# Optimization experiments

Measured on AMD Instinct MI355X. Metric: run time of the kernel, lower is better.

## Reference

```python
import jax, jax.numpy as jnp
import numpy as np

B, T, C, H = 8, 2048, 1024, 64  # batch, seq, n_embed, head_size


def setup_inputs() -> dict:
    key = jax.random.key(0)
    ks = jax.random.split(key, 6)
    k = jax.random.normal(ks[0], (B, T, C), dtype=jnp.float32)
    q = jax.random.normal(ks[1], (B, T, C), dtype=jnp.float32)
    v = jax.random.normal(ks[2], (B, T, C), dtype=jnp.float32)
    mask = jnp.ones((B, T), dtype=jnp.int32)  # key-padding mask (1 = keep)
    # nn.Linear(n_embed, head_size, bias=False) weights: [head_size, n_embed]
    s = 1.0 / np.sqrt(C)
    Wk = jax.random.uniform(ks[3], (H, C), jnp.float32, -s, s)
    Wq = jax.random.uniform(ks[4], (H, C), jnp.float32, -s, s)
    Wv = jax.random.uniform(ks[5], (H, C), jnp.float32, -s, s)
    return {"k": k, "q": q, "v": v, "mask": mask, "Wk": Wk, "Wq": Wq, "Wv": Wv}


def reference(k, q, v, mask, Wk, Wq, Wv):
    Tq = q.shape[1]
    kh = jnp.einsum('btc,hc->bth', k, Wk)   # [B,T,H]
    qh = jnp.einsum('btc,hc->bth', q, Wq)   # [B,T,H]
    vh = jnp.einsum('btc,hc->bth', v, Wv)   # [B,T,H]
    scale = kh.shape[-1] ** -0.5
    wei = jnp.einsum('bqh,bkh->bqk', qh, kh) * scale  # [B,T,T]
    # causal (tril) mask
    tril = jnp.tril(jnp.ones((Tq, Tq), dtype=bool))
    neg_inf = jnp.finfo(wei.dtype).min
    wei = jnp.where(tril[None, :, :], wei, neg_inf)
    # key-padding mask: mask [B,T] -> broadcast over query rows
    wei = jnp.where(mask[:, None, :] != 0, wei, neg_inf)
    wei = jax.nn.softmax(wei, axis=-1)
    # dropout p=0.0 (eval) -> identity
    out = jnp.einsum('bqk,bkh->bqh', wei, vh)  # [B,T,H]
    return out
```

## Files before the change

### kernel.cpp

```cpp
#include <hip/hip_runtime.h>
#include <hip/hip_bf16.h>
#include <math.h>

#define Bn 8
#define Tn 2048
#define Cn 1024
#define Hn 64
#define BTHb ((size_t)Bn * Tn * Hn)
#define WLU  8192
#define WLS  ((size_t)WLU * 8)

typedef __attribute__((ext_vector_type(8))) short bf16x8;
typedef __attribute__((ext_vector_type(4))) float f32x4;

static __device__ __forceinline__ unsigned short bf16rne(float f) {
    union { float f; unsigned u; } x; x.f = f;
    return (unsigned short)((x.u + 0x7FFFu + ((x.u >> 16) & 1u)) >> 16);
}

static __device__ __forceinline__ unsigned short hwbf16(float f) {
    union { __hip_bfloat16 h; unsigned short u; } c;
    c.h = __float2bfloat16(f);
    return c.u;
}

static __device__ __forceinline__ bf16x8 cvt8(const float4 a, const float4 b) {
    bf16x8 r;
    r[0] = (short)hwbf16(a.x); r[1] = (short)hwbf16(a.y);
    r[2] = (short)hwbf16(a.z); r[3] = (short)hwbf16(a.w);
    r[4] = (short)hwbf16(b.x); r[5] = (short)hwbf16(b.y);
    r[6] = (short)hwbf16(b.z); r[7] = (short)hwbf16(b.w);
    return r;
}

__global__ __launch_bounds__(256) void wconv_kernel(
    const float* __restrict__ Wk, const float* __restrict__ Wq,
    const float* __restrict__ Wv, unsigned short* __restrict__ WL)
{
    const int which = blockIdx.y;
    const float* W = (which == 0) ? Wk : (which == 1) ? Wq : Wv;
    unsigned short* dst = WL + (size_t)which * WLS;
    const int tid = threadIdx.x;
#pragma unroll
    for (int i = 0; i < 4; ++i) {
        const int u    = blockIdx.x * 1024 + i * 256 + tid;
        const int kc32 = u >> 8;
        const int ht   = (u >> 6) & 3;
        const int l    = u & 63;
        const float* wp =
            W + (size_t)(ht * 16 + (l & 15)) * Cn + kc32 * 32 + (l >> 4) * 8;
        const float4 a = *(const float4*)wp;
        const float4 b = *(const float4*)(wp + 4);
        *(bf16x8*)&dst[(size_t)u * 8] = cvt8(a, b);
    }
}

__global__ __launch_bounds__(256, 4) void proj_kernel(
    const float* __restrict__ k, const float* __restrict__ q,
    const float* __restrict__ v,
    const unsigned short* __restrict__ WL,
    unsigned short* __restrict__ ws)
{
    const int which = blockIdx.y;
    const float* X = (which == 0) ? k : (which == 1) ? q : v;
    const unsigned short* WLm = WL + (size_t)which * WLS;
    unsigned short* O = ws + (size_t)which * BTHb;

    __shared__ __align__(16) float smem[8192];
    unsigned short* Xbf = (unsigned short*)smem;

    const int tid  = threadIdx.x;
    const int wave = __builtin_amdgcn_readfirstlane(tid >> 6);
    const int lane = tid & 63;
    const int m    = lane & 15;
    const int quad = lane >> 4;
    const int row0 = blockIdx.x * 16;

    const float* Xt = X + (size_t)row0 * Cn + tid * 4;
#pragma unroll
    for (int p = 0; p < 16; ++p) {
        const float4 xv = *(const float4*)(Xt + (size_t)p * Cn);
        ushort4 xb;
        xb.x = hwbf16(xv.x); xb.y = hwbf16(xv.y);
        xb.z = hwbf16(xv.z); xb.w = hwbf16(xv.w);
        const int pu = (tid >> 1) ^ (p & 7);
        *(ushort4*)&Xbf[p * 1024 + pu * 8 + (tid & 1) * 4] = xb;
    }
    __syncthreads();

    f32x4 acc[4];
#pragma unroll
    for (int t = 0; t < 4; ++t) acc[t] = (f32x4){0.f, 0.f, 0.f, 0.f};

#pragma unroll
    for (int cc = 0; cc < 8; ++cc) {
        const int c  = wave * 8 + cc;
        const int pu = (c * 4 + quad) ^ (m & 7);
        const bf16x8 a = *(const bf16x8*)&Xbf[m * 1024 + pu * 8];
#pragma unroll
        for (int ht = 0; ht < 4; ++ht) {
            const bf16x8 bfr =
                *(const bf16x8*)&WLm[(size_t)((c * 4 + ht) * 64 + lane) * 8];
            acc[ht] = __builtin_amdgcn_mfma_f32_16x16x32_bf16(
                a, bfr, acc[ht], 0, 0, 0);
        }
    }

    __syncthreads();
    float (*Rs)[64][17] = (float (*)[64][17])smem;
    if (wave > 0) {
#pragma unroll
        for (int ht = 0; ht < 4; ++ht)
#pragma unroll
            for (int r = 0; r < 4; ++r)
                Rs[wave - 1][lane][ht * 4 + r] = acc[ht][r];
    }
    __syncthreads();
    if (wave == 0) {
#pragma unroll
        for (int w = 0; w < 3; ++w)
#pragma unroll
            for (int ht = 0; ht < 4; ++ht)
#pragma unroll
                for (int r = 0; r < 4; ++r)
                    acc[ht][r] += Rs[w][lane][ht * 4 + r];

#pragma unroll
        for (int ht = 0; ht < 4; ++ht)
#pragma unroll
            for (int r = 0; r < 4; ++r)
                O[(size_t)(row0 + quad * 4 + r) * Hn + ht * 16 + m] =
                    bf16rne(acc[ht][r]);
    }
}

__global__ __launch_bounds__(256) void attn_kernel(
    const unsigned short* __restrict__ ws,
    const int* __restrict__ mask,
    float* __restrict__ out)
{
    const unsigned short* kh = ws;
    const unsigned short* qh = ws + BTHb;
    const unsigned short* vh = ws + 2 * BTHb;

    const int b   = blockIdx.y;
    const int qt  = blockIdx.x;
    const int tid = threadIdx.x;
    const int wave = __builtin_amdgcn_readfirstlane(tid >> 6);
    const int lane = tid & 63;
    const int ln   = lane & 15;
    const int quad = lane >> 4;

    __shared__ unsigned short Ks[64][72];
    __shared__ unsigned short Vt[64][72];
    __shared__ unsigned short Ps[64][72];
    __shared__ int Msk[64];

    const int wrb = qt * 64 + wave * 16;

    bf16x8 qa[2];
#pragma unroll
    for (int kc = 0; kc < 2; ++kc)
        qa[kc] = *(const bf16x8*)(qh + ((size_t)b * Tn + wrb + ln) * Hn
                                     + kc * 32 + quad * 8);

    f32x4 oacc[4];
#pragma unroll
    for (int t = 0; t < 4; ++t) oacc[t] = (f32x4){0.f, 0.f, 0.f, 0.f};
    float mrow[4] = {-1e30f, -1e30f, -1e30f, -1e30f};
    float lrow[4] = {0.f, 0.f, 0.f, 0.f};

    const int krow = tid >> 2, kseg = tid & 3;
    const int vcol = tid & 63, vseg = tid >> 6;

    uint4 kreg[2], vreg[2];
    int mreg = 0;
    {
        const unsigned short* kp =
            kh + ((size_t)b * Tn + krow) * Hn + kseg * 16;
        kreg[0] = *(const uint4*)kp;
        kreg[1] = *(const uint4*)(kp + 8);
        const unsigned short* vp =
            vh + ((size_t)b * Tn + vcol) * Hn + vseg * 16;
        vreg[0] = *(const uint4*)vp;
        vreg[1] = *(const uint4*)(vp + 8);
        if (tid < 64) mreg = mask[(size_t)b * Tn + tid];
    }

    for (int j = 0; j <= qt; ++j) {
        __syncthreads();
        *(uint4*)&Ks[krow][kseg * 16]     = kreg[0];
        *(uint4*)&Ks[krow][kseg * 16 + 8] = kreg[1];
        {
            const unsigned short* vs = (const unsigned short*)vreg;
#pragma unroll
            for (int jj = 0; jj < 16; ++jj)
                Vt[vseg * 16 + jj][vcol] = vs[jj];
        }
        if (tid < 64) Msk[tid] = mreg;
        __syncthreads();

        if (j < qt) {
            const unsigned short* kp =
                kh + ((size_t)b * Tn + (j + 1) * 64 + krow) * Hn + kseg * 16;
            kreg[0] = *(const uint4*)kp;
            kreg[1] = *(const uint4*)(kp + 8);
            const unsigned short* vp =
                vh + ((size_t)b * Tn + (j + 1) * 64 + vcol) * Hn + vseg * 16;
            vreg[0] = *(const uint4*)vp;
            vreg[1] = *(const uint4*)(vp + 8);
            if (tid < 64) mreg = mask[(size_t)b * Tn + (j + 1) * 64 + tid];
        }

        f32x4 sacc[4];
#pragma unroll
        for (int t = 0; t < 4; ++t) sacc[t] = (f32x4){0.f, 0.f, 0.f, 0.f};
#pragma unroll
        for (int kc = 0; kc < 2; ++kc) {
#pragma unroll
            for (int nt = 0; nt < 4; ++nt) {
                const bf16x8 kb =
                    *(const bf16x8*)&Ks[nt * 16 + ln][kc * 32 + quad * 8];
                sacc[nt] = __builtin_amdgcn_mfma_f32_16x16x32_bf16(
                    qa[kc], kb, sacc[nt], 0, 0, 0);
            }
        }

        const bool fullv = (j < qt);
        float pv[4][4];
        float mt[4] = {-1e30f, -1e30f, -1e30f, -1e30f};
#pragma unroll
        for (int nt = 0; nt < 4; ++nt) {
            const bool mk = (Msk[nt * 16 + ln] != 0);
            const int kpos = j * 64 + nt * 16 + ln;
#pragma unroll
            for (int r = 0; r < 4; ++r) {
                float s = sacc[nt][r] * 0.125f;
                const bool valid =
                    mk && (fullv || kpos <= wrb + quad * 4 + r);
                s = valid ? s : -1e30f;
                pv[nt][r] = s;
                mt[r] = fmaxf(mt[r], s);
            }
        }
#pragma unroll
        for (int r = 0; r < 4; ++r) {
            mt[r] = fmaxf(mt[r], __shfl_xor(mt[r], 1));
            mt[r] = fmaxf(mt[r], __shfl_xor(mt[r], 2));
            mt[r] = fmaxf(mt[r], __shfl_xor(mt[r], 4));
            mt[r] = fmaxf(mt[r], __shfl_xor(mt[r], 8));
        }
        float alpha[4], rsum[4];
#pragma unroll
        for (int r = 0; r < 4; ++r) {
            const float mn = fmaxf(mrow[r], mt[r]);
            alpha[r] = __expf(mrow[r] - mn);
            mrow[r] = mn;
            rsum[r] = 0.f;
        }
#pragma unroll
        for (int nt = 0; nt < 4; ++nt)
#pragma unroll
            for (int r = 0; r < 4; ++r) {
                const float p = (pv[nt][r] <= -1e29f)
                                    ? 0.f
                                    : __expf(pv[nt][r] - mrow[r]);
                pv[nt][r] = p;
                rsum[r] += p;
            }
#pragma unroll
        for (int r = 0; r < 4; ++r) {
            rsum[r] += __shfl_xor(rsum[r], 1);
            rsum[r] += __shfl_xor(rsum[r], 2);
            rsum[r] += __shfl_xor(rsum[r], 4);
            rsum[r] += __shfl_xor(rsum[r], 8);
            lrow[r] = lrow[r] * alpha[r] + rsum[r];
        }
#pragma unroll
        for (int nt = 0; nt < 4; ++nt)
#pragma unroll
            for (int r = 0; r < 4; ++r) oacc[nt][r] *= alpha[r];

#pragma unroll
        for (int nt = 0; nt < 4; ++nt)
#pragma unroll
            for (int r = 0; r < 4; ++r)
                Ps[wave * 16 + quad * 4 + r][nt * 16 + ln] =
                    bf16rne(pv[nt][r]);
        asm volatile("s_waitcnt lgkmcnt(0)" ::: "memory");

#pragma unroll
        for (int kc = 0; kc < 2; ++kc) {
            const bf16x8 pa =
                *(const bf16x8*)&Ps[wave * 16 + ln][kc * 32 + quad * 8];
#pragma unroll
            for (int nt = 0; nt < 4; ++nt) {
                const bf16x8 vb =
                    *(const bf16x8*)&Vt[nt * 16 + ln][kc * 32 + quad * 8];
                oacc[nt] = __builtin_amdgcn_mfma_f32_16x16x32_bf16(
                    pa, vb, oacc[nt], 0, 0, 0);
            }
        }
    }

#pragma unroll
    for (int r = 0; r < 4; ++r) {
        const float inv = 1.0f / lrow[r];
        const size_t rowoff = ((size_t)b * Tn + wrb + quad * 4 + r) * Hn;
#pragma unroll
        for (int nt = 0; nt < 4; ++nt)
            out[rowoff + nt * 16 + ln] = oacc[nt][r] * inv;
    }
}

extern "C" void kernel_launch(void* const* d_in, const int* in_sizes, int n_in,
                              void* d_out, int out_size, void* d_ws, size_t ws_size,
                              hipStream_t stream)
{
    const float* k    = (const float*)d_in[0];
    const float* q    = (const float*)d_in[1];
    const float* v    = (const float*)d_in[2];
    const int*   mask = (const int*)d_in[3];
    const float* Wk   = (const float*)d_in[4];
    const float* Wq   = (const float*)d_in[5];
    const float* Wv   = (const float*)d_in[6];
    float* out = (float*)d_out;
    unsigned short* ws = (unsigned short*)d_ws;

    unsigned short* WL = (unsigned short*)d_out;

    dim3 wb(256), wg(8, 3);
    wconv_kernel<<<wg, wb, 0, stream>>>(Wk, Wq, Wv, WL);

    dim3 pb(256), pg(Bn * Tn / 16, 3);
    proj_kernel<<<pg, pb, 0, stream>>>(k, q, v, WL, ws);

    dim3 ab(256), ag(Tn / 64, Bn);
    attn_kernel<<<ag, ab, 0, stream>>>(ws, mask, out);
}
```

Before: 278.4 us.

## Split attention into 32-row query tiles with heavy-first block ordering

The attention kernel now uses 128-thread blocks, each handling 32 query rows instead of 64, giving 512 blocks laid out on a 1D grid. Blocks are ordered so the longest causal tiles launch first and the batch index varies fastest. K/V staging is redone for half as many threads, each loading 32 elements. The goal is better load balance and occupancy across the causal triangle, at the cost of loading each K/V tile twice as often overall.

After: 278.9 us. No clear change (+0.2%).

```diff
diff --git a/kernel.cpp b/kernel.cpp
--- a/kernel.cpp
+++ b/kernel.cpp
@@ -134,7 +134,7 @@
     }
 }
 
-__global__ __launch_bounds__(256) void attn_kernel(
+__global__ __launch_bounds__(128, 2) void attn_kernel(
     const unsigned short* __restrict__ ws,
     const int* __restrict__ mask,
     float* __restrict__ out)
@@ -143,8 +143,8 @@
     const unsigned short* qh = ws + BTHb;
     const unsigned short* vh = ws + 2 * BTHb;
 
-    const int b   = blockIdx.y;
-    const int qt  = blockIdx.x;
+    const int b   = blockIdx.x & 7;
+    const int j   = 63 - (blockIdx.x >> 3);
     const int tid = threadIdx.x;
     const int wave = __builtin_amdgcn_readfirstlane(tid >> 6);
     const int lane = tid & 63;
@@ -153,10 +153,11 @@
 
     __shared__ unsigned short Ks[64][72];
     __shared__ unsigned short Vt[64][72];
-    __shared__ unsigned short Ps[64][72];
+    __shared__ unsigned short Ps[32][72];
     __shared__ int Msk[64];
 
-    const int wrb = qt * 64 + wave * 16;
+    const int ntile = (j >> 1) + 1;
+    const int wrb = j * 32 + wave * 16;
 
     bf16x8 qa[2];
 #pragma unroll
@@ -170,46 +171,56 @@
     float mrow[4] = {-1e30f, -1e30f, -1e30f, -1e30f};
     float lrow[4] = {0.f, 0.f, 0.f, 0.f};
 
-    const int krow = tid >> 2, kseg = tid & 3;
+    const int krow = tid >> 1, kseg = tid & 1;
     const int vcol = tid & 63, vseg = tid >> 6;
 
-    uint4 kreg[2], vreg[2];
+    uint4 kreg[4], vreg[4];
     int mreg = 0;
     {
         const unsigned short* kp =
-            kh + ((size_t)b * Tn + krow) * Hn + kseg * 16;
+            kh + ((size_t)b * Tn + krow) * Hn + kseg * 32;
         kreg[0] = *(const uint4*)kp;
         kreg[1] = *(const uint4*)(kp + 8);
+        kreg[2] = *(const uint4*)(kp + 16);
+        kreg[3] = *(const uint4*)(kp + 24);
         const unsigned short* vp =
-            vh + ((size_t)b * Tn + vcol) * Hn + vseg * 16;
+            vh + ((size_t)b * Tn + vcol) * Hn + vseg * 32;
         vreg[0] = *(const uint4*)vp;
         vreg[1] = *(const uint4*)(vp + 8);
+        vreg[2] = *(const uint4*)(vp + 16);
+        vreg[3] = *(const uint4*)(vp + 24);
         if (tid < 64) mreg = mask[(size_t)b * Tn + tid];
     }
 
-    for (int j = 0; j <= qt; ++j) {
+    for (int jj = 0; jj < ntile; ++jj) {
         __syncthreads();
-        *(uint4*)&Ks[krow][kseg * 16]     = kreg[0];
-        *(uint4*)&Ks[krow][kseg * 16 + 8] = kreg[1];
+        *(uint4*)&Ks[krow][kseg * 32]      = kreg[0];
+        *(uint4*)&Ks[krow][kseg * 32 + 8]  = kreg[1];
+        *(uint4*)&Ks[krow][kseg * 32 + 16] = kreg[2];
+        *(uint4*)&Ks[krow][kseg * 32 + 24] = kreg[3];
         {
             const unsigned short* vs = (const unsigned short*)vreg;
 #pragma unroll
-            for (int jj = 0; jj < 16; ++jj)
-                Vt[vseg * 16 + jj][vcol] = vs[jj];
+            for (int dd = 0; dd < 32; ++dd)
+                Vt[vseg * 32 + dd][vcol] = vs[dd];
         }
         if (tid < 64) Msk[tid] = mreg;
         __syncthreads();
 
-        if (j < qt) {
-            const unsigned short* kp =
-                kh + ((size_t)b * Tn + (j + 1) * 64 + krow) * Hn + kseg * 16;
+        if (jj + 1 < ntile) {
+            const unsigned short* kp = kh +
+                ((size_t)b * Tn + (jj + 1) * 64 + krow) * Hn + kseg * 32;
             kreg[0] = *(const uint4*)kp;
             kreg[1] = *(const uint4*)(kp + 8);
-            const unsigned short* vp =
-                vh + ((size_t)b * Tn + (j + 1) * 64 + vcol) * Hn + vseg * 16;
+            kreg[2] = *(const uint4*)(kp + 16);
+            kreg[3] = *(const uint4*)(kp + 24);
+            const unsigned short* vp = vh +
+                ((size_t)b * Tn + (jj + 1) * 64 + vcol) * Hn + vseg * 32;
             vreg[0] = *(const uint4*)vp;
             vreg[1] = *(const uint4*)(vp + 8);
-            if (tid < 64) mreg = mask[(size_t)b * Tn + (j + 1) * 64 + tid];
+            vreg[2] = *(const uint4*)(vp + 16);
+            vreg[3] = *(const uint4*)(vp + 24);
+            if (tid < 64) mreg = mask[(size_t)b * Tn + (jj + 1) * 64 + tid];
         }
 
         f32x4 sacc[4];
@@ -226,13 +237,13 @@
             }
         }
 
-        const bool fullv = (j < qt);
+        const bool fullv = (64 * (jj + 1) <= 32 * j);
         float pv[4][4];
         float mt[4] = {-1e30f, -1e30f, -1e30f, -1e30f};
 #pragma unroll
         for (int nt = 0; nt < 4; ++nt) {
             const bool mk = (Msk[nt * 16 + ln] != 0);
-            const int kpos = j * 64 + nt * 16 + ln;
+            const int kpos = jj * 64 + nt * 16 + ln;
 #pragma unroll
             for (int r = 0; r < 4; ++r) {
                 float s = sacc[nt][r] * 0.125f;
@@ -335,6 +346,6 @@
     dim3 pb(256), pg(Bn * Tn / 16, 3);
     proj_kernel<<<pg, pb, 0, stream>>>(k, q, v, WL, ws);
 
-    dim3 ab(256), ag(Tn / 64, Bn);
+    dim3 ab(128), ag(512);
     attn_kernel<<<ag, ab, 0, stream>>>(ws, mask, out);
 }
```
